# Kernel optimization log

Measured on AMD Instinct MI355X. Metric: run time of the kernel, lower is better.

## Reference

```python
import jax, jax.numpy as jnp
import numpy as np

T_THRESHOLD = 1e-4      # VolumeRenderer T_threshold / composite_test_fw threshold
NEAR_DISTANCE = 0.01    # hparams.NEAR_DISTANCE clamp applied to hits_t


def setup_inputs() -> dict:
    key = jax.random.key(0)
    k1, k2, k3 = jax.random.split(key, 3)
    N_rays, N_samples = 65536, 256
    rays = jax.random.normal(k1, (N_rays, 6), dtype=jnp.float32)
    # sigmas are NN outputs (post-activation densities >= 0)
    sigmas = 2.0 * jax.random.uniform(k2, (N_rays, N_samples), dtype=jnp.float32)
    rgbs = jax.random.uniform(k3, (N_rays, N_samples, 3), dtype=jnp.float32)
    center = jnp.zeros((3,), dtype=jnp.float32)
    half_size = jnp.ones((3,), dtype=jnp.float32)
    return {"rays": rays, "sigmas": sigmas, "rgbs": rgbs,
            "center": center, "half_size": half_size}


def reference(rays, sigmas, rgbs, center, half_size):
    N_samples = sigmas.shape[1]
    rays_o = rays[:, 0:3]                      # (R, 3)
    rays_d = rays[:, 3:6]
    rays_d = rays_d / (jnp.linalg.norm(rays_d, axis=-1, keepdims=True) + 1e-8)

    # --- RayAABBIntersector: slab test against the scene box ---
    safe_d = jnp.where(jnp.abs(rays_d) > 1e-8, rays_d, 1e-8)
    inv_d = 1.0 / safe_d
    t1 = (center - half_size - rays_o) * inv_d
    t2 = (center + half_size - rays_o) * inv_d
    tmin = jnp.max(jnp.minimum(t1, t2), axis=-1)   # (R,)
    tmax = jnp.min(jnp.maximum(t1, t2), axis=-1)
    hit = tmax > jnp.maximum(tmin, 0.0)
    near = jnp.maximum(tmin, 0.0)
    # forward(): clamp near bound below NEAR_DISTANCE
    near = jnp.where(hit & (near < NEAR_DISTANCE), NEAR_DISTANCE, near)
    far = jnp.where(hit, tmax, near)

    # --- RayMarcher: uniform marching between near/far (padded, masked) ---
    delta = (far - near) / N_samples                               # (R,)
    offs = (jnp.arange(N_samples, dtype=jnp.float32) + 0.5)
    ts = near[:, None] + offs[None, :] * delta[:, None]            # (R, S)

    # --- VolumeRenderer: front-to-back compositing with T_threshold stop ---
    sd = sigmas * delta[:, None]                                   # sigma * dt
    # exclusive transmittance: T_i = exp(-sum_{j<i} sigma_j dt_j)
    T = jnp.exp(-(jnp.cumsum(sd, axis=1) - sd))
    alpha = 1.0 - jnp.exp(-sd)
    alive = (T >= T_THRESHOLD) & hit[:, None]
    ws = jnp.where(alive, alpha * T, 0.0)                          # (R, S)

    opacity = jnp.sum(ws, axis=1)                                  # (R,)
    rgb = jnp.einsum('rs,rsc->rc', ws, rgbs)                       # (R, 3)
    # exp_step_factor != 0 (aabb > 0.5) -> black background
    rgb_bg = jnp.zeros((3,), dtype=rgb.dtype)
    rgb = rgb + rgb_bg * (1.0 - opacity)[:, None]
    return rgb
```

## Files before the change

### kernel.cpp

```cpp
#include <hip/hip_runtime.h>
#include <math.h>

#define N_RAYS 65536
#define N_SAMPLES 256
#define T_THRESHOLD 1e-4f
#define NEAR_DISTANCE 0.01f

__global__ __launch_bounds__(256) void ngp_render_kernel(
    const float* __restrict__ rays,
    const float* __restrict__ sigmas,
    const float* __restrict__ rgbs,
    const float* __restrict__ center,
    const float* __restrict__ half_size,
    float* __restrict__ out)
{
    const int gtid = blockIdx.x * blockDim.x + threadIdx.x;
    const int ray  = gtid >> 6;
    const int lane = threadIdx.x & 63;
    if (ray >= N_RAYS) return;

    const float* rp = rays + (size_t)ray * 6;
    float o[3] = { rp[0], rp[1], rp[2] };
    float d[3] = { rp[3], rp[4], rp[5] };
    float inv_norm = 1.0f / (sqrtf(d[0]*d[0] + d[1]*d[1] + d[2]*d[2]) + 1e-8f);
    d[0] *= inv_norm; d[1] *= inv_norm; d[2] *= inv_norm;

    float tmin = -INFINITY, tmax = INFINITY;
    #pragma unroll
    for (int a = 0; a < 3; ++a) {
        float da  = (fabsf(d[a]) > 1e-8f) ? d[a] : 1e-8f;
        float inv = 1.0f / da;
        float t1  = (center[a] - half_size[a] - o[a]) * inv;
        float t2  = (center[a] + half_size[a] - o[a]) * inv;
        tmin = fmaxf(tmin, fminf(t1, t2));
        tmax = fminf(tmax, fmaxf(t1, t2));
    }
    const bool hit = tmax > fmaxf(tmin, 0.0f);

    if (!hit) {
        if (lane == 0) {
            float* op = out + (size_t)ray * 3;
            op[0] = 0.0f; op[1] = 0.0f; op[2] = 0.0f;
        }
        return;
    }

    float near = fmaxf(tmin, 0.0f);
    if (near < NEAR_DISTANCE) near = NEAR_DISTANCE;
    const float far   = tmax;
    const float delta = (far - near) * (1.0f / (float)N_SAMPLES);

    const float4 sg = *reinterpret_cast<const float4*>(
        sigmas + (size_t)ray * N_SAMPLES + lane * 4);
    const float sd0 = sg.x * delta;
    const float sd1 = sg.y * delta;
    const float sd2 = sg.z * delta;
    const float sd3 = sg.w * delta;
    const float p0 = sd0;
    const float p1 = p0 + sd1;
    const float p2 = p1 + sd2;
    const float p3 = p2 + sd3;

    float incl = p3;
    #pragma unroll
    for (int off = 1; off < 64; off <<= 1) {
        float v = __shfl_up(incl, off, 64);
        if (lane >= off) incl += v;
    }
    const float excl = incl - p3;

    const float T0 = expf(-excl);
    const float T1 = expf(-(excl + p0));
    const float T2 = expf(-(excl + p1));
    const float T3 = expf(-(excl + p2));
    const float a0 = 1.0f - expf(-sd0);
    const float a1 = 1.0f - expf(-sd1);
    const float a2 = 1.0f - expf(-sd2);
    const float a3 = 1.0f - expf(-sd3);
    const float ws0 = (T0 >= T_THRESHOLD) ? a0 * T0 : 0.0f;
    const float ws1 = (T1 >= T_THRESHOLD) ? a1 * T1 : 0.0f;
    const float ws2 = (T2 >= T_THRESHOLD) ? a2 * T2 : 0.0f;
    const float ws3 = (T3 >= T_THRESHOLD) ? a3 * T3 : 0.0f;

    const float* rb = rgbs + (size_t)ray * N_SAMPLES * 3 + (size_t)lane * 12;
    const float4 r0 = *reinterpret_cast<const float4*>(rb + 0);
    const float4 r1 = *reinterpret_cast<const float4*>(rb + 4);
    const float4 r2 = *reinterpret_cast<const float4*>(rb + 8);
    float R = ws0 * r0.x + ws1 * r0.w + ws2 * r1.z + ws3 * r2.y;
    float G = ws0 * r0.y + ws1 * r1.x + ws2 * r1.w + ws3 * r2.z;
    float B = ws0 * r0.z + ws1 * r1.y + ws2 * r2.x + ws3 * r2.w;

    #pragma unroll
    for (int off = 32; off > 0; off >>= 1) {
        R += __shfl_xor(R, off, 64);
        G += __shfl_xor(G, off, 64);
        B += __shfl_xor(B, off, 64);
    }
    if (lane == 0) {
        float* op = out + (size_t)ray * 3;
        op[0] = R; op[1] = G; op[2] = B;
    }
}

extern "C" void kernel_launch(void* const* d_in, const int* in_sizes, int n_in,
                              void* d_out, int out_size, void* d_ws, size_t ws_size,
                              hipStream_t stream) {
    const float* rays      = (const float*)d_in[0];
    const float* sigmas    = (const float*)d_in[1];
    const float* rgbs      = (const float*)d_in[2];
    const float* center    = (const float*)d_in[3];
    const float* half_size = (const float*)d_in[4];
    float* out = (float*)d_out;

    const int threads = 256;
    const int blocks  = N_RAYS / 4;
    ngp_render_kernel<<<blocks, threads, 0, stream>>>(
        rays, sigmas, rgbs, center, half_size, out);
}
```

Before: 28.72 us.

## Compact hit rays into a list and render only hits with persistent waves

A setup kernel runs the ray-box test once per ray, writes zeros for rays that miss, and appends hit rays and their step size to a workspace list through an atomic counter. A persistent-grid render kernel then walks only the compacted hit list, one wave per ray, so no waves are launched for rays that miss. In exchange it adds a memset, a second kernel launch and a global atomic per hit ray, and rays are visited in scattered order. It falls back to the original one-pass kernel when the workspace is too small.

```diff
diff --git a/kernel.cpp b/kernel.cpp
--- a/kernel.cpp
+++ b/kernel.cpp
@@ -6,20 +6,16 @@
 #define T_THRESHOLD 1e-4f
 #define NEAR_DISTANCE 0.01f
 
-__global__ __launch_bounds__(256) void ngp_render_kernel(
-    const float* __restrict__ rays,
-    const float* __restrict__ sigmas,
-    const float* __restrict__ rgbs,
+#define WS_LIST_OFF   16
+#define WS_DELTA_OFF  (16 + 4 * N_RAYS)
+#define WS_NEEDED     (16 + 8 * N_RAYS)
+
+__device__ __forceinline__ void ray_aabb(
+    const float* __restrict__ rp,
     const float* __restrict__ center,
     const float* __restrict__ half_size,
-    float* __restrict__ out)
-{
-    const int gtid = blockIdx.x * blockDim.x + threadIdx.x;
-    const int ray  = gtid >> 6;
-    const int lane = threadIdx.x & 63;
-    if (ray >= N_RAYS) return;
-
-    const float* rp = rays + (size_t)ray * 6;
+    bool& hit, float& delta)
+{
     float o[3] = { rp[0], rp[1], rp[2] };
     float d[3] = { rp[3], rp[4], rp[5] };
     float inv_norm = 1.0f / (sqrtf(d[0]*d[0] + d[1]*d[1] + d[2]*d[2]) + 1e-8f);
@@ -35,7 +31,123 @@
         tmin = fmaxf(tmin, fminf(t1, t2));
         tmax = fminf(tmax, fmaxf(t1, t2));
     }
-    const bool hit = tmax > fmaxf(tmin, 0.0f);
+    hit = tmax > fmaxf(tmin, 0.0f);
+    float near = fmaxf(tmin, 0.0f);
+    if (hit && near < NEAR_DISTANCE) near = NEAR_DISTANCE;
+    const float far = hit ? tmax : near;
+    delta = (far - near) * (1.0f / (float)N_SAMPLES);
+}
+
+__global__ __launch_bounds__(256) void ngp_setup_kernel(
+    const float* __restrict__ rays,
+    const float* __restrict__ center,
+    const float* __restrict__ half_size,
+    float* __restrict__ out,
+    unsigned int* __restrict__ counter,
+    int* __restrict__ list,
+    float* __restrict__ deltas)
+{
+    const int ray = blockIdx.x * blockDim.x + threadIdx.x;
+    if (ray >= N_RAYS) return;
+
+    bool hit; float delta;
+    ray_aabb(rays + (size_t)ray * 6, center, half_size, hit, delta);
+
+    if (!hit) {
+        float* op = out + (size_t)ray * 3;
+        op[0] = 0.0f; op[1] = 0.0f; op[2] = 0.0f;
+    } else {
+        deltas[ray] = delta;
+        const unsigned int pos = atomicAdd(counter, 1u);
+        list[pos] = ray;
+    }
+}
+
+__global__ __launch_bounds__(256) void ngp_render_kernel(
+    const float* __restrict__ sigmas,
+    const float* __restrict__ rgbs,
+    float* __restrict__ out,
+    const unsigned int* __restrict__ counter,
+    const int* __restrict__ list,
+    const float* __restrict__ deltas)
+{
+    const int lane    = threadIdx.x & 63;
+    const int waveId  = (blockIdx.x * blockDim.x + threadIdx.x) >> 6;
+    const int nWaves  = (gridDim.x * blockDim.x) >> 6;
+    const unsigned int count = *counter;
+
+    for (unsigned int w = waveId; w < count; w += nWaves) {
+        const int   ray   = list[w];
+        const float delta = deltas[ray];
+
+        const float4 sg = *reinterpret_cast<const float4*>(
+            sigmas + (size_t)ray * N_SAMPLES + lane * 4);
+        const float sd0 = sg.x * delta;
+        const float sd1 = sg.y * delta;
+        const float sd2 = sg.z * delta;
+        const float sd3 = sg.w * delta;
+        const float p0 = sd0;
+        const float p1 = p0 + sd1;
+        const float p2 = p1 + sd2;
+        const float p3 = p2 + sd3;
+
+        float incl = p3;
+        #pragma unroll
+        for (int off = 1; off < 64; off <<= 1) {
+            float v = __shfl_up(incl, off, 64);
+            if (lane >= off) incl += v;
+        }
+        const float excl = incl - p3;
+
+        const float T0 = expf(-excl);
+        const float T1 = expf(-(excl + p0));
+        const float T2 = expf(-(excl + p1));
+        const float T3 = expf(-(excl + p2));
+        const float a0 = 1.0f - expf(-sd0);
+        const float a1 = 1.0f - expf(-sd1);
+        const float a2 = 1.0f - expf(-sd2);
+        const float a3 = 1.0f - expf(-sd3);
+        const float ws0 = (T0 >= T_THRESHOLD) ? a0 * T0 : 0.0f;
+        const float ws1 = (T1 >= T_THRESHOLD) ? a1 * T1 : 0.0f;
+        const float ws2 = (T2 >= T_THRESHOLD) ? a2 * T2 : 0.0f;
+        const float ws3 = (T3 >= T_THRESHOLD) ? a3 * T3 : 0.0f;
+
+        const float* rb = rgbs + (size_t)ray * N_SAMPLES * 3 + (size_t)lane * 12;
+        const float4 r0 = *reinterpret_cast<const float4*>(rb + 0);
+        const float4 r1 = *reinterpret_cast<const float4*>(rb + 4);
+        const float4 r2 = *reinterpret_cast<const float4*>(rb + 8);
+        float R = ws0 * r0.x + ws1 * r0.w + ws2 * r1.z + ws3 * r2.y;
+        float G = ws0 * r0.y + ws1 * r1.x + ws2 * r1.w + ws3 * r2.z;
+        float B = ws0 * r0.z + ws1 * r1.y + ws2 * r2.x + ws3 * r2.w;
+
+        #pragma unroll
+        for (int off = 32; off > 0; off >>= 1) {
+            R += __shfl_xor(R, off, 64);
+            G += __shfl_xor(G, off, 64);
+            B += __shfl_xor(B, off, 64);
+        }
+        if (lane == 0) {
+            float* op = out + (size_t)ray * 3;
+            op[0] = R; op[1] = G; op[2] = B;
+        }
+    }
+}
+
+__global__ __launch_bounds__(256) void ngp_onepass_kernel(
+    const float* __restrict__ rays,
+    const float* __restrict__ sigmas,
+    const float* __restrict__ rgbs,
+    const float* __restrict__ center,
+    const float* __restrict__ half_size,
+    float* __restrict__ out)
+{
+    const int gtid = blockIdx.x * blockDim.x + threadIdx.x;
+    const int ray  = gtid >> 6;
+    const int lane = threadIdx.x & 63;
+    if (ray >= N_RAYS) return;
+
+    bool hit; float delta;
+    ray_aabb(rays + (size_t)ray * 6, center, half_size, hit, delta);
 
     if (!hit) {
         if (lane == 0) {
@@ -45,21 +157,11 @@
         return;
     }
 
-    float near = fmaxf(tmin, 0.0f);
-    if (near < NEAR_DISTANCE) near = NEAR_DISTANCE;
-    const float far   = tmax;
-    const float delta = (far - near) * (1.0f / (float)N_SAMPLES);
-
     const float4 sg = *reinterpret_cast<const float4*>(
         sigmas + (size_t)ray * N_SAMPLES + lane * 4);
-    const float sd0 = sg.x * delta;
-    const float sd1 = sg.y * delta;
-    const float sd2 = sg.z * delta;
-    const float sd3 = sg.w * delta;
-    const float p0 = sd0;
-    const float p1 = p0 + sd1;
-    const float p2 = p1 + sd2;
-    const float p3 = p2 + sd3;
+    const float sd0 = sg.x * delta, sd1 = sg.y * delta;
+    const float sd2 = sg.z * delta, sd3 = sg.w * delta;
+    const float p0 = sd0, p1 = p0 + sd1, p2 = p1 + sd2, p3 = p2 + sd3;
 
     float incl = p3;
     #pragma unroll
@@ -73,10 +175,8 @@
     const float T1 = expf(-(excl + p0));
     const float T2 = expf(-(excl + p1));
     const float T3 = expf(-(excl + p2));
-    const float a0 = 1.0f - expf(-sd0);
-    const float a1 = 1.0f - expf(-sd1);
-    const float a2 = 1.0f - expf(-sd2);
-    const float a3 = 1.0f - expf(-sd3);
+    const float a0 = 1.0f - expf(-sd0), a1 = 1.0f - expf(-sd1);
+    const float a2 = 1.0f - expf(-sd2), a3 = 1.0f - expf(-sd3);
     const float ws0 = (T0 >= T_THRESHOLD) ? a0 * T0 : 0.0f;
     const float ws1 = (T1 >= T_THRESHOLD) ? a1 * T1 : 0.0f;
     const float ws2 = (T2 >= T_THRESHOLD) ? a2 * T2 : 0.0f;
@@ -112,8 +212,20 @@
     const float* half_size = (const float*)d_in[4];
     float* out = (float*)d_out;
 
-    const int threads = 256;
-    const int blocks  = N_RAYS / 4;
-    ngp_render_kernel<<<blocks, threads, 0, stream>>>(
-        rays, sigmas, rgbs, center, half_size, out);
-}
+    if (ws_size >= (size_t)WS_NEEDED) {
+        unsigned int* counter = (unsigned int*)d_ws;
+        int*   list   = (int*)  ((char*)d_ws + WS_LIST_OFF);
+        float* deltas = (float*)((char*)d_ws + WS_DELTA_OFF);
+
+        hipMemsetAsync(counter, 0, 4, stream);
+
+        ngp_setup_kernel<<<N_RAYS / 256, 256, 0, stream>>>(
+            rays, center, half_size, out, counter, list, deltas);
+
+        ngp_render_kernel<<<2048, 256, 0, stream>>>(
+            sigmas, rgbs, out, counter, list, deltas);
+    } else {
+        ngp_onepass_kernel<<<N_RAYS / 4, 256, 0, stream>>>(
+            rays, sigmas, rgbs, center, half_size, out);
+    }
+}
```

New measurement: 44.84 us. 1.56x slower.

## Process eight rays per wave, compacting hit rays and prefetching next ray

Applied to the files above, without the earlier changes.

Each wave now handles eight rays. The AABB test runs in parallel across the first eight lanes, and a ballot yields the mask of rays that hit the box. The wave loops only over hit rays and loads the next ray's sigma and rgb data while compositing the current one. Missed rays no longer occupy a whole wave, and the prefetch is meant to hide memory latency. In exchange the grid is smaller and each wave does serial work, which lowers the number of independent waves available to hide DRAM latency.

```diff
diff --git a/kernel.cpp b/kernel.cpp
--- a/kernel.cpp
+++ b/kernel.cpp
@@ -5,6 +5,8 @@
 #define N_SAMPLES 256
 #define T_THRESHOLD 1e-4f
 #define NEAR_DISTANCE 0.01f
+#define RAYS_PER_WAVE 8
+#define WAVES_PER_BLOCK 4
 
 __global__ __launch_bounds__(256) void ngp_render_kernel(
     const float* __restrict__ rays,
@@ -14,91 +16,119 @@
     const float* __restrict__ half_size,
     float* __restrict__ out)
 {
-    const int gtid = blockIdx.x * blockDim.x + threadIdx.x;
-    const int ray  = gtid >> 6;
-    const int lane = threadIdx.x & 63;
-    if (ray >= N_RAYS) return;
+    const int lane   = threadIdx.x & 63;
+    const int waveId = (blockIdx.x * blockDim.x + threadIdx.x) >> 6;
+    const int base   = waveId * RAYS_PER_WAVE;
+    if (base >= N_RAYS) return;
 
-    const float* rp = rays + (size_t)ray * 6;
-    float o[3] = { rp[0], rp[1], rp[2] };
-    float d[3] = { rp[3], rp[4], rp[5] };
-    float inv_norm = 1.0f / (sqrtf(d[0]*d[0] + d[1]*d[1] + d[2]*d[2]) + 1e-8f);
-    d[0] *= inv_norm; d[1] *= inv_norm; d[2] *= inv_norm;
+    bool  hit   = false;
+    float delta = 0.0f;
+    if (lane < RAYS_PER_WAVE) {
+        const float* rp = rays + (size_t)(base + lane) * 6;
+        float o[3] = { rp[0], rp[1], rp[2] };
+        float d[3] = { rp[3], rp[4], rp[5] };
+        float inv_norm = 1.0f / (sqrtf(d[0]*d[0] + d[1]*d[1] + d[2]*d[2]) + 1e-8f);
+        d[0] *= inv_norm; d[1] *= inv_norm; d[2] *= inv_norm;
 
-    float tmin = -INFINITY, tmax = INFINITY;
-    #pragma unroll
-    for (int a = 0; a < 3; ++a) {
-        float da  = (fabsf(d[a]) > 1e-8f) ? d[a] : 1e-8f;
-        float inv = 1.0f / da;
-        float t1  = (center[a] - half_size[a] - o[a]) * inv;
-        float t2  = (center[a] + half_size[a] - o[a]) * inv;
-        tmin = fmaxf(tmin, fminf(t1, t2));
-        tmax = fminf(tmax, fmaxf(t1, t2));
-    }
-    const bool hit = tmax > fmaxf(tmin, 0.0f);
-
-    if (!hit) {
-        if (lane == 0) {
-            float* op = out + (size_t)ray * 3;
+        float tmin = -INFINITY, tmax = INFINITY;
+        #pragma unroll
+        for (int a = 0; a < 3; ++a) {
+            float da  = (fabsf(d[a]) > 1e-8f) ? d[a] : 1e-8f;
+            float inv = 1.0f / da;
+            float t1  = (center[a] - half_size[a] - o[a]) * inv;
+            float t2  = (center[a] + half_size[a] - o[a]) * inv;
+            tmin = fmaxf(tmin, fminf(t1, t2));
+            tmax = fminf(tmax, fmaxf(t1, t2));
+        }
+        hit = tmax > fmaxf(tmin, 0.0f);
+        if (hit) {
+            float near = fmaxf(tmin, 0.0f);
+            if (near < NEAR_DISTANCE) near = NEAR_DISTANCE;
+            delta = (tmax - near) * (1.0f / (float)N_SAMPLES);
+        } else {
+            float* op = out + (size_t)(base + lane) * 3;
             op[0] = 0.0f; op[1] = 0.0f; op[2] = 0.0f;
         }
-        return;
     }
 
-    float near = fmaxf(tmin, 0.0f);
-    if (near < NEAR_DISTANCE) near = NEAR_DISTANCE;
-    const float far   = tmax;
-    const float delta = (far - near) * (1.0f / (float)N_SAMPLES);
+    unsigned long long m = __ballot(hit);
+    if (m == 0ull) return;
 
-    const float4 sg = *reinterpret_cast<const float4*>(
-        sigmas + (size_t)ray * N_SAMPLES + lane * 4);
-    const float sd0 = sg.x * delta;
-    const float sd1 = sg.y * delta;
-    const float sd2 = sg.z * delta;
-    const float sd3 = sg.w * delta;
-    const float p0 = sd0;
-    const float p1 = p0 + sd1;
-    const float p2 = p1 + sd2;
-    const float p3 = p2 + sd3;
+    int src = __ffsll((unsigned long long)m) - 1;
+    m &= m - 1;
+    int   ray_n = base + src;
+    float dlt_n = __shfl(delta, src, 64);
+    const float* sp = sigmas + (size_t)ray_n * N_SAMPLES + lane * 4;
+    const float* rb = rgbs   + (size_t)ray_n * N_SAMPLES * 3 + (size_t)lane * 12;
+    float4 sg_n = *reinterpret_cast<const float4*>(sp);
+    float4 r0_n = *reinterpret_cast<const float4*>(rb + 0);
+    float4 r1_n = *reinterpret_cast<const float4*>(rb + 4);
+    float4 r2_n = *reinterpret_cast<const float4*>(rb + 8);
 
-    float incl = p3;
-    #pragma unroll
-    for (int off = 1; off < 64; off <<= 1) {
-        float v = __shfl_up(incl, off, 64);
-        if (lane >= off) incl += v;
-    }
-    const float excl = incl - p3;
+    bool more = true;
+    while (more) {
+        const int    ray_c = ray_n;
+        const float  dlt_c = dlt_n;
+        const float4 sg = sg_n, r0 = r0_n, r1 = r1_n, r2 = r2_n;
 
-    const float T0 = expf(-excl);
-    const float T1 = expf(-(excl + p0));
-    const float T2 = expf(-(excl + p1));
-    const float T3 = expf(-(excl + p2));
-    const float a0 = 1.0f - expf(-sd0);
-    const float a1 = 1.0f - expf(-sd1);
-    const float a2 = 1.0f - expf(-sd2);
-    const float a3 = 1.0f - expf(-sd3);
-    const float ws0 = (T0 >= T_THRESHOLD) ? a0 * T0 : 0.0f;
-    const float ws1 = (T1 >= T_THRESHOLD) ? a1 * T1 : 0.0f;
-    const float ws2 = (T2 >= T_THRESHOLD) ? a2 * T2 : 0.0f;
-    const float ws3 = (T3 >= T_THRESHOLD) ? a3 * T3 : 0.0f;
+        more = (m != 0ull);
+        if (more) {
+            src = __ffsll((unsigned long long)m) - 1;
+            m &= m - 1;
+            ray_n = base + src;
+            dlt_n = __shfl(delta, src, 64);
+            const float* spn = sigmas + (size_t)ray_n * N_SAMPLES + lane * 4;
+            const float* rbn = rgbs   + (size_t)ray_n * N_SAMPLES * 3 + (size_t)lane * 12;
+            sg_n = *reinterpret_cast<const float4*>(spn);
+            r0_n = *reinterpret_cast<const float4*>(rbn + 0);
+            r1_n = *reinterpret_cast<const float4*>(rbn + 4);
+            r2_n = *reinterpret_cast<const float4*>(rbn + 8);
+        }
 
-    const float* rb = rgbs + (size_t)ray * N_SAMPLES * 3 + (size_t)lane * 12;
-    const float4 r0 = *reinterpret_cast<const float4*>(rb + 0);
-    const float4 r1 = *reinterpret_cast<const float4*>(rb + 4);
-    const float4 r2 = *reinterpret_cast<const float4*>(rb + 8);
-    float R = ws0 * r0.x + ws1 * r0.w + ws2 * r1.z + ws3 * r2.y;
-    float G = ws0 * r0.y + ws1 * r1.x + ws2 * r1.w + ws3 * r2.z;
-    float B = ws0 * r0.z + ws1 * r1.y + ws2 * r2.x + ws3 * r2.w;
+        const float sd0 = sg.x * dlt_c;
+        const float sd1 = sg.y * dlt_c;
+        const float sd2 = sg.z * dlt_c;
+        const float sd3 = sg.w * dlt_c;
+        const float p0 = sd0;
+        const float p1 = p0 + sd1;
+        const float p2 = p1 + sd2;
+        const float p3 = p2 + sd3;
 
-    #pragma unroll
-    for (int off = 32; off > 0; off >>= 1) {
-        R += __shfl_xor(R, off, 64);
-        G += __shfl_xor(G, off, 64);
-        B += __shfl_xor(B, off, 64);
-    }
-    if (lane == 0) {
-        float* op = out + (size_t)ray * 3;
-        op[0] = R; op[1] = G; op[2] = B;
+        float incl = p3;
+        #pragma unroll
+        for (int off = 1; off < 64; off <<= 1) {
+            float v = __shfl_up(incl, off, 64);
+            if (lane >= off) incl += v;
+        }
+        const float excl = incl - p3;
+
+        const float T0 = expf(-excl);
+        const float T1 = expf(-(excl + p0));
+        const float T2 = expf(-(excl + p1));
+        const float T3 = expf(-(excl + p2));
+        const float a0 = 1.0f - expf(-sd0);
+        const float a1 = 1.0f - expf(-sd1);
+        const float a2 = 1.0f - expf(-sd2);
+        const float a3 = 1.0f - expf(-sd3);
+        const float ws0 = (T0 >= T_THRESHOLD) ? a0 * T0 : 0.0f;
+        const float ws1 = (T1 >= T_THRESHOLD) ? a1 * T1 : 0.0f;
+        const float ws2 = (T2 >= T_THRESHOLD) ? a2 * T2 : 0.0f;
+        const float ws3 = (T3 >= T_THRESHOLD) ? a3 * T3 : 0.0f;
+
+        float R = ws0 * r0.x + ws1 * r0.w + ws2 * r1.z + ws3 * r2.y;
+        float G = ws0 * r0.y + ws1 * r1.x + ws2 * r1.w + ws3 * r2.z;
+        float B = ws0 * r0.z + ws1 * r1.y + ws2 * r2.x + ws3 * r2.w;
+
+        #pragma unroll
+        for (int off = 32; off > 0; off >>= 1) {
+            R += __shfl_xor(R, off, 64);
+            G += __shfl_xor(G, off, 64);
+            B += __shfl_xor(B, off, 64);
+        }
+        if (lane == 0) {
+            float* op = out + (size_t)ray_c * 3;
+            op[0] = R; op[1] = G; op[2] = B;
+        }
     }
 }
 
@@ -112,8 +142,8 @@
     const float* half_size = (const float*)d_in[4];
     float* out = (float*)d_out;
 
-    const int threads = 256;
-    const int blocks  = N_RAYS / 4;
-    ngp_render_kernel<<<blocks, threads, 0, stream>>>(
+    const int raysPerBlock = RAYS_PER_WAVE * WAVES_PER_BLOCK;
+    const int blocks = N_RAYS / raysPerBlock;
+    ngp_render_kernel<<<blocks, 256, 0, stream>>>(
         rays, sigmas, rgbs, center, half_size, out);
 }
```

New measurement: 30.37 us. 5.8% more time.
